# Kernel tuning notes

Hardware: AMD Instinct MI355X
Metric: run time of the kernel (lower is better)

Reference implementation:

```python
import jax, jax.numpy as jnp
import numpy as np

NUM_PAIRS, PAIR_DIM, MACRO_DIM, NUM_SLOTS, BATCH = 28, 128, 256, 64, 4096
D_ALL = NUM_PAIRS * PAIR_DIM  # 3584
EPS = 1e-5


def _layernorm(x, g, b):
    mu = jnp.mean(x, axis=-1, keepdims=True)
    var = jnp.mean(jnp.square(x - mu), axis=-1, keepdims=True)
    return (x - mu) * jax.lax.rsqrt(var + EPS) * g + b


def _memory_read(q, keys, values):
    # attention-style associative read: softmax(q K^T / sqrt(dk)) V
    dk = keys.shape[-1]
    scores = jnp.einsum('bd,sd->bs', q, keys) / jnp.sqrt(jnp.asarray(dk, q.dtype))
    attn = jax.nn.softmax(scores, axis=-1)
    return jnp.einsum('bs,sv->bv', attn, values)


def setup_inputs() -> dict:
    key = jax.random.key(0)
    ks = jax.random.split(key, 12)
    s = lambda k, shape, scale=0.02: jax.random.normal(k, shape, dtype=jnp.float32) * scale
    return {
        'pair_states': jax.random.normal(ks[0], (BATCH, NUM_PAIRS, PAIR_DIM), dtype=jnp.float32),
        'macro_state': jax.random.normal(ks[1], (BATCH, MACRO_DIM), dtype=jnp.float32),
        'mem_pair_keys': s(ks[2], (NUM_SLOTS, PAIR_DIM)),
        'mem_pair_vals': s(ks[3], (NUM_SLOTS, D_ALL)),
        'mem_macro_keys': s(ks[4], (NUM_SLOTS, MACRO_DIM)),
        'mem_macro_vals': s(ks[5], (NUM_SLOTS, D_ALL)),
        'fusion_w1': s(ks[6], (2 * D_ALL, D_ALL)),
        'fusion_b1': jnp.zeros((D_ALL,), jnp.float32),
        'fusion_ln_g': jnp.ones((D_ALL,), jnp.float32),
        'fusion_ln_b': jnp.zeros((D_ALL,), jnp.float32),
        'fusion_w2': s(ks[7], (D_ALL, D_ALL)),
        'fusion_b2': jnp.zeros((D_ALL,), jnp.float32),
        'pair_w': s(ks[8], (NUM_PAIRS, 2 * PAIR_DIM, PAIR_DIM)),
        'pair_b': jnp.zeros((NUM_PAIRS, PAIR_DIM), jnp.float32),
        'pair_ln_g': jnp.ones((NUM_PAIRS, PAIR_DIM), jnp.float32),
        'pair_ln_b': jnp.zeros((NUM_PAIRS, PAIR_DIM), jnp.float32),
    }


def reference(pair_states, macro_state, mem_pair_keys, mem_pair_vals,
              mem_macro_keys, mem_macro_vals, fusion_w1, fusion_b1,
              fusion_ln_g, fusion_ln_b, fusion_w2, fusion_b2,
              pair_w, pair_b, pair_ln_g, pair_ln_b):
    B = pair_states.shape[0]
    # associative memory reads
    pair_query = jnp.mean(pair_states, axis=1)                       # (B, pair_dim)
    pair_corr = _memory_read(pair_query, mem_pair_keys, mem_pair_vals)   # (B, D_ALL)
    macro_corr = _memory_read(macro_state, mem_macro_keys, mem_macro_vals)  # (B, D_ALL)
    # fusion MLP: Linear -> LayerNorm -> GELU -> Linear
    h = jnp.concatenate([pair_corr, macro_corr], axis=-1) @ fusion_w1 + fusion_b1
    h = jax.nn.gelu(_layernorm(h, fusion_ln_g, fusion_ln_b), approximate=False)
    fused = (h @ fusion_w2 + fusion_b2).reshape(B, NUM_PAIRS, PAIR_DIM)
    # per-pair Linear + LayerNorm, batched over the pair axis
    x = jnp.concatenate([pair_states, fused], axis=-1)               # (B, P, 2*pair_dim)
    out = jnp.einsum('bpd,pde->bpe', x, pair_w) + pair_b
    return _layernorm(out, pair_ln_g, pair_ln_b)
```

## Files before the change

kernel.cpp:

```cpp
#include <hip/hip_runtime.h>
#include <hip/hip_bf16.h>
#include <math.h>


#define B_SZ  4096
#define NPAIR 28
#define PDIM  128
#define MDIM  256
#define NSLOT 64
#define DALL  3584
#define DCAT  7168
#define KS2   16
#define KCH2  448

typedef __hip_bfloat16 bf16;
typedef __attribute__((ext_vector_type(8))) short bf16x8;
typedef __attribute__((ext_vector_type(4))) float f32x4;

#define BARRIER() asm volatile("s_barrier" ::: "memory")
#define LGKM0()   asm volatile("s_waitcnt lgkmcnt(0)" ::: "memory")
#define VMCNT4()  asm volatile("s_waitcnt vmcnt(4)" ::: "memory")
#define VMCNT0()  asm volatile("s_waitcnt vmcnt(0)" ::: "memory")

__device__ __forceinline__ void async_copy16(void* lds, const void* g) {
  __builtin_amdgcn_global_load_lds((__attribute__((address_space(1))) void*)g,
                                   (__attribute__((address_space(3))) void*)lds,
                                   16, 0, 0);
}

__global__ __launch_bounds__(512, 2)
void gemm224(const bf16* __restrict__ A, const bf16* __restrict__ Bt,
             bf16* __restrict__ Cout, const float* __restrict__ bias) {
  __shared__ __align__(16) char smem[131072];
  const int tid = threadIdx.x;
  const int wid = tid >> 6, lane = tid & 63;
  const int lr = lane & 15, lk = lane >> 4;
  const int wm = wid >> 1, wn = wid & 1;
  const int swz = ((int)blockIdx.x & 7) * 32 + ((int)blockIdx.x >> 3);
  const int bx = swz & 15, by = swz >> 4;
  const int col0 = bx * 224, row0 = by * 256;

  char* sA = smem;
  char* sB = smem + 65536;

  const int srow = tid >> 3;
  const int sg = (tid & 7) ^ (srow & 7);
  const bf16* aStage = A + (long)(row0 + srow) * DALL + sg * 8;
  const bf16* bStage = Bt + (long)(col0 + srow) * DALL + sg * 8;
  const int wOff = wid << 10;

  const int NT = DALL >> 6;

  const int sx = lr & 7;
  const int arowb = wm * 64 + lr;
  const int browb = wn * 112 + lr;

  f32x4 acc[4][7];
  const f32x4 zero = {0.f, 0.f, 0.f, 0.f};
#pragma unroll
  for (int m = 0; m < 4; ++m)
#pragma unroll
    for (int n = 0; n < 7; ++n) acc[m][n] = zero;

#pragma unroll
  for (int i = 0; i < 4; ++i)
    async_copy16(sB + i * 8192 + wOff, bStage + (long)i * 64 * DALL);
#pragma unroll
  for (int i = 0; i < 4; ++i)
    async_copy16(sA + i * 8192 + wOff, aStage + (long)i * 64 * DALL);
#pragma unroll
  for (int i = 0; i < 4; ++i)
    async_copy16(sB + 32768 + i * 8192 + wOff, bStage + (long)i * 64 * DALL + 64);
  VMCNT4();
  BARRIER();

  bf16x8 af[4][2], bf[7][2];

  for (int t = 0; t < NT; ++t) {
    const int cur = t & 1;
    char* cA = sA + cur * 32768;
    char* cB = sB + cur * 32768;
    char* nA = sA + (cur ^ 1) * 32768;

    if (t + 1 < NT) {
      const bf16* g = aStage + (long)(t + 1) * 64;
#pragma unroll
      for (int i = 0; i < 4; ++i)
        async_copy16(nA + i * 8192 + wOff, g + (long)i * 64 * DALL);
    }
#pragma unroll
    for (int m = 0; m < 4; ++m)
#pragma unroll
      for (int kk = 0; kk < 2; ++kk)
        af[m][kk] = *(const bf16x8*)(cA + (arowb + m * 16) * 128 +
                                     ((((kk << 2) | lk) ^ sx) << 4));
#pragma unroll
    for (int n = 0; n < 7; ++n)
#pragma unroll
      for (int kk = 0; kk < 2; ++kk)
        bf[n][kk] = *(const bf16x8*)(cB + (browb + n * 16) * 128 +
                                     ((((kk << 2) | lk) ^ sx) << 4));
    __builtin_amdgcn_s_setprio(1);
#pragma unroll
    for (int m = 0; m < 4; ++m)
#pragma unroll
      for (int n = 0; n < 4; ++n)
#pragma unroll
        for (int kk = 0; kk < 2; ++kk)
          acc[m][n] = __builtin_amdgcn_mfma_f32_16x16x32_bf16(
              af[m][kk], bf[n][kk], acc[m][n], 0, 0, 0);
    __builtin_amdgcn_s_setprio(0);
    LGKM0();
    BARRIER();

    const int more = (t + 2 < NT);
    if (more) {
      const bf16* g = bStage + (long)(t + 2) * 64;
#pragma unroll
      for (int i = 0; i < 4; ++i)
        async_copy16(cB + i * 8192 + wOff, g + (long)i * 64 * DALL);
    }
    __builtin_amdgcn_s_setprio(1);
#pragma unroll
    for (int m = 0; m < 4; ++m)
#pragma unroll
      for (int n = 4; n < 7; ++n)
#pragma unroll
        for (int kk = 0; kk < 2; ++kk)
          acc[m][n] = __builtin_amdgcn_mfma_f32_16x16x32_bf16(
              af[m][kk], bf[n][kk], acc[m][n], 0, 0, 0);
    __builtin_amdgcn_s_setprio(0);
    if (more) { VMCNT4(); } else { VMCNT0(); }
    BARRIER();
  }

#pragma unroll
  for (int m = 0; m < 4; ++m) {
#pragma unroll
    for (int n = 0; n < 7; ++n) {
      const int gc = col0 + wn * 112 + n * 16 + lr;
      const float bia = bias[gc];
#pragma unroll
      for (int j = 0; j < 4; ++j) {
        const int gr = row0 + wm * 64 + m * 16 + lk * 4 + j;
        Cout[(long)gr * DALL + gc] = __float2bfloat16(acc[m][n][j] + bia);
      }
    }
  }
}

__global__ __launch_bounds__(256)
void tconv_kernel(const float* __restrict__ in, bf16* __restrict__ out,
                  int R, int C, int inBatch, int outBatch) {
  __shared__ float tile[32][33];
  const int tid = threadIdx.x;
  const int tx = tid & 31, ty = tid >> 5;
  const long ib = (long)blockIdx.z * inBatch;
  const long ob = (long)blockIdx.z * outBatch;
  const int c0 = blockIdx.x * 32, r0 = blockIdx.y * 32;
#pragma unroll
  for (int i = 0; i < 4; ++i)
    tile[ty + i * 8][tx] = in[ib + (long)(r0 + ty + i * 8) * C + c0 + tx];
  __syncthreads();
#pragma unroll
  for (int i = 0; i < 4; ++i)
    out[ob + (long)(c0 + ty + i * 8) * R + r0 + tx] =
        __float2bfloat16(tile[tx][ty + i * 8]);
}

__global__ __launch_bounds__(256)
void conv2_kernel(const float* __restrict__ pv, const float* __restrict__ mv,
                  bf16* __restrict__ pvb, bf16* __restrict__ mvb) {
  const float* in = blockIdx.y ? mv : pv;
  bf16* out = blockIdx.y ? mvb : pvb;
  const int i = (blockIdx.x * 256 + threadIdx.x) * 8;
  float4 a = *(const float4*)(in + i);
  float4 b = *(const float4*)(in + i + 4);
  bf16 o[8];
  o[0] = __float2bfloat16(a.x); o[1] = __float2bfloat16(a.y);
  o[2] = __float2bfloat16(a.z); o[3] = __float2bfloat16(a.w);
  o[4] = __float2bfloat16(b.x); o[5] = __float2bfloat16(b.y);
  o[6] = __float2bfloat16(b.z); o[7] = __float2bfloat16(b.w);
  *(bf16x8*)(out + i) = *(bf16x8*)o;
}

__global__ __launch_bounds__(256)
void prep_kernel(const float* __restrict__ ps, const float* __restrict__ mac,
                 const float* __restrict__ pkeys, const float* __restrict__ mkeys,
                 bf16* __restrict__ psb, bf16* __restrict__ att) {
  const int b = blockIdx.x, tid = threadIdx.x;
  __shared__ float q[PDIM];
  __shared__ float mrow[MDIM];
  const float* prow = ps + (long)b * DALL;
  if (tid < MDIM) mrow[tid] = mac[(long)b * MDIM + tid];
  if (tid < PDIM) {
    float s = 0.f;
#pragma unroll
    for (int p = 0; p < NPAIR; ++p) s += prow[p * PDIM + tid];
    q[tid] = s * (1.f / NPAIR);
  }
  for (int i = tid; i < DALL; i += 256)
    psb[(long)b * DALL + i] = __float2bfloat16(prow[i]);
  __syncthreads();
  const int wid = tid >> 6, lane = tid & 63;
  if (wid == 0) {
    float sc = 0.f;
    const float* kr = pkeys + lane * PDIM;
    for (int d = 0; d < PDIM; ++d) sc += q[d] * kr[d];
    sc *= 0.08838834764831845f;
    float mx = sc;
#pragma unroll
    for (int m = 32; m; m >>= 1) mx = fmaxf(mx, __shfl_xor(mx, m));
    float e = expf(sc - mx);
    float ssum = e;
#pragma unroll
    for (int m = 32; m; m >>= 1) ssum += __shfl_xor(ssum, m);
    att[(long)b * 128 + lane] = __float2bfloat16(e / ssum);
  } else if (wid == 1) {
    float sc = 0.f;
    const float* kr = mkeys + lane * MDIM;
    for (int d = 0; d < MDIM; ++d) sc += mrow[d] * kr[d];
    sc *= 0.0625f;
    float mx = sc;
#pragma unroll
    for (int m = 32; m; m >>= 1) mx = fmaxf(mx, __shfl_xor(mx, m));
    float e = expf(sc - mx);
    float ssum = e;
#pragma unroll
    for (int m = 32; m; m >>= 1) ssum += __shfl_xor(ssum, m);
    att[(long)b * 128 + 64 + lane] = __float2bfloat16(e / ssum);
  }
}

__global__ __launch_bounds__(256)
void precompute_direct(const float* __restrict__ w1, const bf16* __restrict__ pvb,
                       const bf16* __restrict__ mvb, float* __restrict__ part) {
  __shared__ __align__(16) bf16 sAt[256 * 40];
  __shared__ __align__(16) bf16 sBt[64 * 32];
  const int tid = threadIdx.x, wid = tid >> 6, lane = tid & 63;
  const int lr = lane & 15, lk = lane >> 4;
  const int n0 = blockIdx.x * 256;
  const int ksb = blockIdx.y;
  const int kbase = ksb * KCH2;
  const bf16* vb = (ksb < 8) ? pvb : mvb;
  const int kcol0 = (ksb < 8) ? kbase : kbase - DALL;

  const int bs = tid >> 2;
  const int bgs = (tid & 3) ^ (bs & 3);

  f32x4 acc[4][4];
  const f32x4 zero = {0.f, 0.f, 0.f, 0.f};
#pragma unroll
  for (int m = 0; m < 4; ++m)
#pragma unroll
    for (int n = 0; n < 4; ++n) acc[m][n] = zero;

  for (int kt = 0; kt < KCH2; kt += 32) {
    __syncthreads();
    {
      const float* src = w1 + (long)(kbase + kt) * DALL + n0 + tid;
      bf16* dst = sAt + tid * 40;
#pragma unroll
      for (int r = 0; r < 32; ++r)
        dst[r] = __float2bfloat16(src[(long)r * DALL]);
    }
    async_copy16((char*)sBt + tid * 16,
                 vb + (long)bs * DALL + kcol0 + kt + bgs * 8);
    __syncthreads();
    bf16x8 af[4], bfr[4];
#pragma unroll
    for (int m = 0; m < 4; ++m)
      af[m] = *(const bf16x8*)((const char*)sAt +
                               ((wid * 64 + m * 16 + lr) * 40 + lk * 8) * 2);
#pragma unroll
    for (int n = 0; n < 4; ++n) {
      const int s = n * 16 + lr;
      bfr[n] = *(const bf16x8*)((const char*)sBt + s * 64 + ((lk ^ (s & 3)) << 4));
    }
#pragma unroll
    for (int m = 0; m < 4; ++m)
#pragma unroll
      for (int n = 0; n < 4; ++n)
        acc[m][n] =
            __builtin_amdgcn_mfma_f32_16x16x32_bf16(af[m], bfr[n], acc[m][n], 0, 0, 0);
  }
#pragma unroll
  for (int m = 0; m < 4; ++m)
#pragma unroll
    for (int n = 0; n < 4; ++n)
#pragma unroll
      for (int j = 0; j < 4; ++j) {
        const int gn = n0 + wid * 64 + m * 16 + lk * 4 + j;
        const int s = n * 16 + lr;
        part[((long)ksb * DALL + gn) * 64 + s] = acc[m][n][j];
      }
}

__global__ __launch_bounds__(256)
void reduce_cvt(const float* __restrict__ part, bf16* __restrict__ cvt) {
  const long i4 = ((long)blockIdx.x * 256 + threadIdx.x) * 4;
  const int n = (int)(i4 >> 7), sc = (int)(i4 & 127);
  const int half = sc >> 6, s0 = sc & 63;
  f32x4 s = {0.f, 0.f, 0.f, 0.f};
#pragma unroll
  for (int j = 0; j < 8; ++j)
    s += *(const f32x4*)(part + ((long)(half * 8 + j) * DALL + n) * 64 + s0);
#pragma unroll
  for (int k = 0; k < 4; ++k) cvt[i4 + k] = __float2bfloat16(s[k]);
}

template <int OUT_BF16, int ADD_BIAS>
__global__ __launch_bounds__(256)
void gemm_bt(const bf16* __restrict__ A, int lda, const bf16* __restrict__ Bt,
             void* __restrict__ Cout, int ldc, int col_off,
             const float* __restrict__ bias, int K) {
  __shared__ __align__(16) bf16 sA[128 * 32];
  __shared__ __align__(16) bf16 sB[128 * 32];
  const int tid = threadIdx.x;
  const int wid = tid >> 6, lane = tid & 63;
  const int lr = lane & 15, lk = lane >> 4;
  const int col0 = blockIdx.x * 128, row0 = blockIdx.y * 128;
  const int wrow = (wid >> 1) * 64, wcol = (wid & 1) * 64;
  const int ea = tid * 8;
  const int ra = ea >> 5, ca = ea & 31;

  f32x4 acc[4][4];
  const f32x4 zero = {0.f, 0.f, 0.f, 0.f};
#pragma unroll
  for (int m = 0; m < 4; ++m)
#pragma unroll
    for (int n = 0; n < 4; ++n) acc[m][n] = zero;

  const long aBase = (long)row0 * lda;
  const long bBase = (long)col0 * K;
  char* sAb = (char*)sA;
  char* sBb = (char*)sB;
  const int wOff = wid * 1024;

  for (int kt = 0; kt < K; kt += 32) {
    __syncthreads();
#pragma unroll
    for (int i = 0; i < 2; ++i) {
      async_copy16(sAb + i * 4096 + wOff,
                   A + aBase + (long)(ra + i * 64) * lda + kt + ca);
      async_copy16(sBb + i * 4096 + wOff,
                   Bt + bBase + (long)(ra + i * 64) * K + kt + ca);
    }
    __syncthreads();
    bf16x8 af[4], bfr[4];
    const bf16x8* pA = (const bf16x8*)sA;
    const bf16x8* pB = (const bf16x8*)sB;
#pragma unroll
    for (int m = 0; m < 4; ++m) af[m] = pA[(wrow + m * 16 + lr) * 4 + lk];
#pragma unroll
    for (int n = 0; n < 4; ++n) bfr[n] = pB[(wcol + n * 16 + lr) * 4 + lk];
#pragma unroll
    for (int m = 0; m < 4; ++m)
#pragma unroll
      for (int n = 0; n < 4; ++n)
        acc[m][n] =
            __builtin_amdgcn_mfma_f32_16x16x32_bf16(af[m], bfr[n], acc[m][n], 0, 0, 0);
  }
#pragma unroll
  for (int m = 0; m < 4; ++m) {
#pragma unroll
    for (int n = 0; n < 4; ++n) {
      const int gcl = col0 + wcol + n * 16 + lr;
      const float bia = ADD_BIAS ? bias[gcl] : 0.f;
#pragma unroll
      for (int j = 0; j < 4; ++j) {
        const int gr = row0 + wrow + m * 16 + lk * 4 + j;
        const float v = acc[m][n][j] + bia;
        const long off = (long)gr * ldc + col_off + gcl;
        if (OUT_BF16)
          ((bf16*)Cout)[off] = __float2bfloat16(v);
        else
          ((float*)Cout)[off] = v;
      }
    }
  }
}

__global__ __launch_bounds__(256)
void ln_gelu_kernel(const bf16* __restrict__ h, const float* __restrict__ g,
                    const float* __restrict__ bb, bf16* __restrict__ h2) {
  const int row = blockIdx.x, tid = threadIdx.x;
  const bf16* x = h + (long)row * DALL;
  float v[14];
  float s1 = 0.f, s2 = 0.f;
#pragma unroll
  for (int i = 0; i < 14; ++i) {
    v[i] = __bfloat162float(x[i * 256 + tid]);
    s1 += v[i];
    s2 += v[i] * v[i];
  }
#pragma unroll
  for (int m = 32; m; m >>= 1) {
    s1 += __shfl_xor(s1, m);
    s2 += __shfl_xor(s2, m);
  }
  __shared__ float r1[4], r2[4];
  const int wid = tid >> 6, lane = tid & 63;
  if (lane == 0) {
    r1[wid] = s1;
    r2[wid] = s2;
  }
  __syncthreads();
  s1 = r1[0] + r1[1] + r1[2] + r1[3];
  s2 = r2[0] + r2[1] + r2[2] + r2[3];
  const float mean = s1 * (1.f / DALL);
  const float var = s2 * (1.f / DALL) - mean * mean;
  const float rstd = rsqrtf(var + 1e-5f);
#pragma unroll
  for (int i = 0; i < 14; ++i) {
    const int c = i * 256 + tid;
    const float y = (v[i] - mean) * rstd * g[c] + bb[c];
    const float ge = 0.5f * y * (1.f + erff(y * 0.7071067811865475f));
    h2[(long)row * DALL + c] = __float2bfloat16(ge);
  }
}

__global__ __launch_bounds__(256)
void pair_final(const bf16* __restrict__ psb, const bf16* __restrict__ fusedb,
                const bf16* __restrict__ pwT, const float* __restrict__ pb,
                const float* __restrict__ lng, const float* __restrict__ lnb,
                float* __restrict__ out) {
  __shared__ __align__(16) bf16 sA[128 * 32];
  __shared__ __align__(16) bf16 sB[128 * 32];
  const int tid = threadIdx.x, wid = tid >> 6, lane = tid & 63;
  const int lr = lane & 15, lk = lane >> 4;
  const int p = blockIdx.y, row0 = blockIdx.x * 128;
  const int ea = tid * 8, ra = ea >> 5, ca = ea & 31;

  f32x4 acc[2][8];
  const f32x4 zero = {0.f, 0.f, 0.f, 0.f};
#pragma unroll
  for (int m = 0; m < 2; ++m)
#pragma unroll
    for (int n = 0; n < 8; ++n) acc[m][n] = zero;

  const bf16* pwp = pwT + (long)p * (PDIM * MDIM);
  char* sAb = (char*)sA;
  char* sBb = (char*)sB;
  const int wOff = wid * 1024;

  for (int kt = 0; kt < MDIM; kt += 32) {
    __syncthreads();
    const bf16* Asrc = (kt < PDIM) ? psb : fusedb;
    const int kc = kt & (PDIM - 1);
#pragma unroll
    for (int i = 0; i < 2; ++i) {
      async_copy16(sAb + i * 4096 + wOff,
                   Asrc + (long)(row0 + ra + i * 64) * DALL + p * PDIM + kc + ca);
      async_copy16(sBb + i * 4096 + wOff, pwp + (ra + i * 64) * MDIM + kt + ca);
    }
    __syncthreads();
    bf16x8 af[2], bfr[8];
    const bf16x8* pA = (const bf16x8*)sA;
    const bf16x8* pB = (const bf16x8*)sB;
#pragma unroll
    for (int m = 0; m < 2; ++m) af[m] = pA[(wid * 32 + m * 16 + lr) * 4 + lk];
#pragma unroll
    for (int n = 0; n < 8; ++n) bfr[n] = pB[(n * 16 + lr) * 4 + lk];
#pragma unroll
    for (int m = 0; m < 2; ++m)
#pragma unroll
      for (int n = 0; n < 8; ++n)
        acc[m][n] =
            __builtin_amdgcn_mfma_f32_16x16x32_bf16(af[m], bfr[n], acc[m][n], 0, 0, 0);
  }
  float g_[8], b_[8], pb_[8];
#pragma unroll
  for (int n = 0; n < 8; ++n) {
    const int c = n * 16 + lr;
    g_[n] = lng[p * PDIM + c];
    b_[n] = lnb[p * PDIM + c];
    pb_[n] = pb[p * PDIM + c];
  }
#pragma unroll
  for (int m = 0; m < 2; ++m) {
#pragma unroll
    for (int j = 0; j < 4; ++j) {
      float vv[8];
      float s1 = 0.f, s2 = 0.f;
#pragma unroll
      for (int n = 0; n < 8; ++n) {
        vv[n] = acc[m][n][j] + pb_[n];
        s1 += vv[n];
        s2 += vv[n] * vv[n];
      }
#pragma unroll
      for (int msk = 1; msk <= 8; msk <<= 1) {
        s1 += __shfl_xor(s1, msk);
        s2 += __shfl_xor(s2, msk);
      }
      const float mean = s1 * (1.f / 128.f);
      const float var = s2 * (1.f / 128.f) - mean * mean;
      const float rstd = rsqrtf(var + 1e-5f);
      const int gr = row0 + wid * 32 + m * 16 + lk * 4 + j;
      float* orow = out + ((long)gr * NPAIR + p) * PDIM;
#pragma unroll
      for (int n = 0; n < 8; ++n)
        orow[n * 16 + lr] = (vv[n] - mean) * rstd * g_[n] + b_[n];
    }
  }
}

extern "C" void kernel_launch(void* const* d_in, const int* in_sizes, int n_in,
                              void* d_out, int out_size, void* d_ws, size_t ws_size,
                              hipStream_t stream) {
  (void)in_sizes; (void)n_in; (void)out_size; (void)ws_size;
  const float* ps   = (const float*)d_in[0];
  const float* mac  = (const float*)d_in[1];
  const float* pkey = (const float*)d_in[2];
  const float* pval = (const float*)d_in[3];
  const float* mkey = (const float*)d_in[4];
  const float* mval = (const float*)d_in[5];
  const float* w1   = (const float*)d_in[6];
  const float* b1   = (const float*)d_in[7];
  const float* lng1 = (const float*)d_in[8];
  const float* lnb1 = (const float*)d_in[9];
  const float* w2   = (const float*)d_in[10];
  const float* b2   = (const float*)d_in[11];
  const float* pw   = (const float*)d_in[12];
  const float* pb   = (const float*)d_in[13];
  const float* plng = (const float*)d_in[14];
  const float* plnb = (const float*)d_in[15];
  float* out = (float*)d_out;

  char* w = (char*)d_ws;
  size_t off = 0;
  auto carve = [&](size_t bytes) {
    char* pp = w + off;
    off += (bytes + 255) & ~(size_t)255;
    return pp;
  };
  bf16* psb   = (bf16*)carve((size_t)B_SZ * DALL * 2);
  bf16* w2t   = (bf16*)carve((size_t)(DALL + 32) * DALL * 2);
  bf16* pvb   = (bf16*)carve((size_t)NSLOT * DALL * 2);
  bf16* mvb   = (bf16*)carve((size_t)NSLOT * DALL * 2);
  bf16* pwTb  = (bf16*)carve((size_t)NPAIR * PDIM * MDIM * 2);
  bf16* att   = (bf16*)carve((size_t)B_SZ * 128 * 2);
  bf16* cvt   = (bf16*)carve((size_t)DALL * 128 * 2);
  float* part = (float*)carve((size_t)KS2 * DALL * 64 * 4);
  bf16* hpreb = (bf16*)carve((size_t)B_SZ * DALL * 2);
  bf16* h2    = (bf16*)carve((size_t)B_SZ * DALL * 2);
  bf16* fusedb = hpreb;

  conv2_kernel<<<dim3(NSLOT * DALL / 2048, 2), 256, 0, stream>>>(pval, mval, pvb, mvb);
  tconv_kernel<<<dim3(DALL / 32, DALL / 32, 1), 256, 0, stream>>>(w2, w2t, DALL, DALL, 0, 0);
  tconv_kernel<<<dim3(PDIM / 32, MDIM / 32, NPAIR), 256, 0, stream>>>(
      pw, pwTb, MDIM, PDIM, MDIM * PDIM, MDIM * PDIM);
  prep_kernel<<<dim3(B_SZ), 256, 0, stream>>>(ps, mac, pkey, mkey, psb, att);
  precompute_direct<<<dim3(DALL / 256, KS2), 256, 0, stream>>>(w1, pvb, mvb, part);
  reduce_cvt<<<dim3(DALL * 128 / 1024), 256, 0, stream>>>(part, cvt);
  gemm_bt<1, 1><<<dim3(DALL / 128, B_SZ / 128), 256, 0, stream>>>(
      att, 128, cvt, hpreb, DALL, 0, b1, 128);
  ln_gelu_kernel<<<dim3(B_SZ), 256, 0, stream>>>(hpreb, lng1, lnb1, h2);
  gemm224<<<dim3(256), 512, 0, stream>>>(h2, w2t, fusedb, b2);
  pair_final<<<dim3(B_SZ / 128, NPAIR), 256, 0, stream>>>(
      psb, fusedb, pwTb, pb, plng, plnb, out);
}
```

Before: 283.9 us.

## Vectorize bf16 stores and use 64-wide swizzled K tiles in thin GEMMs

Several conversion kernels (tconv, prep, precompute_direct's LDS fill) now pack bf16 values and write 8- or 16-byte vectors instead of scalar 2-byte stores. The generic gemm_bt for the K=128 attention-times-correction GEMM is replaced by a specialized gemm_thin using 64-wide K tiles with an XOR-swizzled LDS layout, halving the number of barrier-separated iterations. pair_final gets the same 64-wide swizzled tiling. The aim is fewer memory transactions, fewer LDS bank conflicts and less synchronization overhead, at the cost of larger LDS footprint per block.

```diff
diff --git a/kernel.cpp b/kernel.cpp
--- a/kernel.cpp
+++ b/kernel.cpp
@@ -15,6 +15,7 @@
 
 typedef __hip_bfloat16 bf16;
 typedef __attribute__((ext_vector_type(8))) short bf16x8;
+typedef __attribute__((ext_vector_type(4))) short short4v;
 typedef __attribute__((ext_vector_type(4))) float f32x4;
 
 #define BARRIER() asm volatile("s_barrier" ::: "memory")
@@ -162,10 +163,11 @@
   for (int i = 0; i < 4; ++i)
     tile[ty + i * 8][tx] = in[ib + (long)(r0 + ty + i * 8) * C + c0 + tx];
   __syncthreads();
-#pragma unroll
-  for (int i = 0; i < 4; ++i)
-    out[ob + (long)(c0 + ty + i * 8) * R + r0 + tx] =
-        __float2bfloat16(tile[tx][ty + i * 8]);
+  const int cl = tid >> 3, rq = (tid & 7) * 4;
+  union { bf16 h[4]; short4v v; } u;
+#pragma unroll
+  for (int j = 0; j < 4; ++j) u.h[j] = __float2bfloat16(tile[rq + j][cl]);
+  *(short4v*)(out + ob + (long)(c0 + cl) * R + r0 + rq) = u.v;
 }
 
 __global__ __launch_bounds__(256)
@@ -176,12 +178,12 @@
   const int i = (blockIdx.x * 256 + threadIdx.x) * 8;
   float4 a = *(const float4*)(in + i);
   float4 b = *(const float4*)(in + i + 4);
-  bf16 o[8];
-  o[0] = __float2bfloat16(a.x); o[1] = __float2bfloat16(a.y);
-  o[2] = __float2bfloat16(a.z); o[3] = __float2bfloat16(a.w);
-  o[4] = __float2bfloat16(b.x); o[5] = __float2bfloat16(b.y);
-  o[6] = __float2bfloat16(b.z); o[7] = __float2bfloat16(b.w);
-  *(bf16x8*)(out + i) = *(bf16x8*)o;
+  union { bf16 h[8]; bf16x8 v; } u;
+  u.h[0] = __float2bfloat16(a.x); u.h[1] = __float2bfloat16(a.y);
+  u.h[2] = __float2bfloat16(a.z); u.h[3] = __float2bfloat16(a.w);
+  u.h[4] = __float2bfloat16(b.x); u.h[5] = __float2bfloat16(b.y);
+  u.h[6] = __float2bfloat16(b.z); u.h[7] = __float2bfloat16(b.w);
+  *(bf16x8*)(out + i) = u.v;
 }
 
 __global__ __launch_bounds__(256)
@@ -199,8 +201,16 @@
     for (int p = 0; p < NPAIR; ++p) s += prow[p * PDIM + tid];
     q[tid] = s * (1.f / NPAIR);
   }
-  for (int i = tid; i < DALL; i += 256)
-    psb[(long)b * DALL + i] = __float2bfloat16(prow[i]);
+  for (int i = tid * 8; i < DALL; i += 2048) {
+    float4 a = *(const float4*)(prow + i);
+    float4 c = *(const float4*)(prow + i + 4);
+    union { bf16 h[8]; bf16x8 v; } u;
+    u.h[0] = __float2bfloat16(a.x); u.h[1] = __float2bfloat16(a.y);
+    u.h[2] = __float2bfloat16(a.z); u.h[3] = __float2bfloat16(a.w);
+    u.h[4] = __float2bfloat16(c.x); u.h[5] = __float2bfloat16(c.y);
+    u.h[6] = __float2bfloat16(c.z); u.h[7] = __float2bfloat16(c.w);
+    *(bf16x8*)(psb + (long)b * DALL + i) = u.v;
+  }
   __syncthreads();
   const int wid = tid >> 6, lane = tid & 63;
   if (wid == 0) {
@@ -261,8 +271,13 @@
       const float* src = w1 + (long)(kbase + kt) * DALL + n0 + tid;
       bf16* dst = sAt + tid * 40;
 #pragma unroll
-      for (int r = 0; r < 32; ++r)
-        dst[r] = __float2bfloat16(src[(long)r * DALL]);
+      for (int r8 = 0; r8 < 32; r8 += 4) {
+        union { bf16 h[4]; short4v v; } u;
+#pragma unroll
+        for (int j = 0; j < 4; ++j)
+          u.h[j] = __float2bfloat16(src[(long)(r8 + j) * DALL]);
+        *(short4v*)(dst + r8) = u.v;
+      }
     }
     async_copy16((char*)sBt + tid * 16,
                  vb + (long)bs * DALL + kcol0 + kt + bgs * 8);
@@ -309,73 +324,64 @@
   for (int k = 0; k < 4; ++k) cvt[i4 + k] = __float2bfloat16(s[k]);
 }
 
-template <int OUT_BF16, int ADD_BIAS>
-__global__ __launch_bounds__(256)
-void gemm_bt(const bf16* __restrict__ A, int lda, const bf16* __restrict__ Bt,
-             void* __restrict__ Cout, int ldc, int col_off,
-             const float* __restrict__ bias, int K) {
-  __shared__ __align__(16) bf16 sA[128 * 32];
-  __shared__ __align__(16) bf16 sB[128 * 32];
-  const int tid = threadIdx.x;
-  const int wid = tid >> 6, lane = tid & 63;
+__global__ __launch_bounds__(256)
+void gemm_thin(const bf16* __restrict__ att, const bf16* __restrict__ cvt,
+               bf16* __restrict__ hpre, const float* __restrict__ bias) {
+  __shared__ __align__(16) bf16 sA[128 * 64];
+  __shared__ __align__(16) bf16 sB[128 * 64];
+  const int tid = threadIdx.x, wid = tid >> 6, lane = tid & 63;
   const int lr = lane & 15, lk = lane >> 4;
   const int col0 = blockIdx.x * 128, row0 = blockIdx.y * 128;
-  const int wrow = (wid >> 1) * 64, wcol = (wid & 1) * 64;
-  const int ea = tid * 8;
-  const int ra = ea >> 5, ca = ea & 31;
-
-  f32x4 acc[4][4];
+  const int srl = lane >> 3;
+  const int sgl = (lane & 7) ^ srl;
+  const int sx = lr & 7;
+
+  f32x4 acc[2][8];
   const f32x4 zero = {0.f, 0.f, 0.f, 0.f};
 #pragma unroll
-  for (int m = 0; m < 4; ++m)
-#pragma unroll
-    for (int n = 0; n < 4; ++n) acc[m][n] = zero;
-
-  const long aBase = (long)row0 * lda;
-  const long bBase = (long)col0 * K;
-  char* sAb = (char*)sA;
-  char* sBb = (char*)sB;
-  const int wOff = wid * 1024;
-
-  for (int kt = 0; kt < K; kt += 32) {
+  for (int m = 0; m < 2; ++m)
+#pragma unroll
+    for (int n = 0; n < 8; ++n) acc[m][n] = zero;
+
+  for (int kt = 0; kt < 2; ++kt) {
     __syncthreads();
 #pragma unroll
-    for (int i = 0; i < 2; ++i) {
-      async_copy16(sAb + i * 4096 + wOff,
-                   A + aBase + (long)(ra + i * 64) * lda + kt + ca);
-      async_copy16(sBb + i * 4096 + wOff,
-                   Bt + bBase + (long)(ra + i * 64) * K + kt + ca);
+    for (int i = 0; i < 4; ++i) {
+      const int r = i * 32 + wid * 8 + srl;
+      async_copy16((char*)sA + i * 4096 + wid * 1024,
+                   att + (long)(row0 + r) * 128 + kt * 64 + sgl * 8);
+      async_copy16((char*)sB + i * 4096 + wid * 1024,
+                   cvt + (long)(col0 + r) * 128 + kt * 64 + sgl * 8);
     }
     __syncthreads();
-    bf16x8 af[4], bfr[4];
-    const bf16x8* pA = (const bf16x8*)sA;
-    const bf16x8* pB = (const bf16x8*)sB;
-#pragma unroll
-    for (int m = 0; m < 4; ++m) af[m] = pA[(wrow + m * 16 + lr) * 4 + lk];
-#pragma unroll
-    for (int n = 0; n < 4; ++n) bfr[n] = pB[(wcol + n * 16 + lr) * 4 + lk];
-#pragma unroll
-    for (int m = 0; m < 4; ++m)
-#pragma unroll
-      for (int n = 0; n < 4; ++n)
-        acc[m][n] =
-            __builtin_amdgcn_mfma_f32_16x16x32_bf16(af[m], bfr[n], acc[m][n], 0, 0, 0);
-  }
-#pragma unroll
-  for (int m = 0; m < 4; ++m) {
-#pragma unroll
-    for (int n = 0; n < 4; ++n) {
-      const int gcl = col0 + wcol + n * 16 + lr;
-      const float bia = ADD_BIAS ? bias[gcl] : 0.f;
+#pragma unroll
+    for (int kk = 0; kk < 2; ++kk) {
+      bf16x8 a0[2], b0[8];
+      const int gb = (((kk << 2) | lk) ^ sx) << 4;
+#pragma unroll
+      for (int m = 0; m < 2; ++m)
+        a0[m] = *(const bf16x8*)((const char*)sA + (wid * 32 + m * 16 + lr) * 128 + gb);
+#pragma unroll
+      for (int n = 0; n < 8; ++n)
+        b0[n] = *(const bf16x8*)((const char*)sB + (n * 16 + lr) * 128 + gb);
+#pragma unroll
+      for (int m = 0; m < 2; ++m)
+#pragma unroll
+        for (int n = 0; n < 8; ++n)
+          acc[m][n] = __builtin_amdgcn_mfma_f32_16x16x32_bf16(
+              a0[m], b0[n], acc[m][n], 0, 0, 0);
+    }
+  }
+#pragma unroll
+  for (int m = 0; m < 2; ++m) {
+#pragma unroll
+    for (int n = 0; n < 8; ++n) {
+      const int gc = col0 + n * 16 + lr;
+      const float bia = bias[gc];
 #pragma unroll
       for (int j = 0; j < 4; ++j) {
-        const int gr = row0 + wrow + m * 16 + lk * 4 + j;
-        const float v = acc[m][n][j] + bia;
-        const long off = (long)gr * ldc + col_off + gcl;
-        if (OUT_BF16)
-          ((bf16*)Cout)[off] = __float2bfloat16(v);
-        else
-          ((float*)Cout)[off] = v;
+        const int gr = row0 + wid * 32 + m * 16 + lk * 4 + j;
+        hpre[(long)gr * DALL + gc] = __float2bfloat16(acc[m][n][j] + bia);
       }
     }
   }
@@ -425,12 +431,15 @@
                 const bf16* __restrict__ pwT, const float* __restrict__ pb,
                 const float* __restrict__ lng, const float* __restrict__ lnb,
                 float* __restrict__ out) {
-  __shared__ __align__(16) bf16 sA[128 * 32];
-  __shared__ __align__(16) bf16 sB[128 * 32];
+  __shared__ __align__(16) bf16 sA[128 * 64];
+  __shared__ __align__(16) bf16 sB[128 * 64];
   const int tid = threadIdx.x, wid = tid >> 6, lane = tid & 63;
   const int lr = lane & 15, lk = lane >> 4;
   const int p = blockIdx.y, row0 = blockIdx.x * 128;
-  const int ea = tid * 8, ra = ea >> 5, ca = ea & 31;
+  const int srl = lane >> 3;
+  const int sgl = (lane & 7) ^ srl;
+  const int sx = lr & 7;
+  const bf16* pwp = pwT + (long)p * (PDIM * MDIM);
 
   f32x4 acc[2][8];
   const f32x4 zero = {0.f, 0.f, 0.f, 0.f};
@@ -439,35 +448,36 @@
 #pragma unroll
     for (int n = 0; n < 8; ++n) acc[m][n] = zero;
 
-  const bf16* pwp = pwT + (long)p * (PDIM * MDIM);
-  char* sAb = (char*)sA;
-  char* sBb = (char*)sB;
-  const int wOff = wid * 1024;
-
-  for (int kt = 0; kt < MDIM; kt += 32) {
+  for (int kt = 0; kt < 4; ++kt) {
     __syncthreads();
-    const bf16* Asrc = (kt < PDIM) ? psb : fusedb;
-    const int kc = kt & (PDIM - 1);
-#pragma unroll
-    for (int i = 0; i < 2; ++i) {
-      async_copy16(sAb + i * 4096 + wOff,
-                   Asrc + (long)(row0 + ra + i * 64) * DALL + p * PDIM + kc + ca);
-      async_copy16(sBb + i * 4096 + wOff, pwp + (ra + i * 64) * MDIM + kt + ca);
+    const bf16* Asrc = (kt < 2) ? psb : fusedb;
+    const int acol = p * PDIM + (kt & 1) * 64;
+#pragma unroll
+    for (int i = 0; i < 4; ++i) {
+      const int r = i * 32 + wid * 8 + srl;
+      async_copy16((char*)sA + i * 4096 + wid * 1024,
+                   Asrc + (long)(row0 + r) * DALL + acol + sgl * 8);
+      async_copy16((char*)sB + i * 4096 + wid * 1024,
+                   pwp + (long)r * MDIM + kt * 64 + sgl * 8);
     }
     __syncthreads();
-    bf16x8 af[2], bfr[8];
-    const bf16x8* pA = (const bf16x8*)sA;
-    const bf16x8* pB = (const bf16x8*)sB;
-#pragma unroll
-    for (int m = 0; m < 2; ++m) af[m] = pA[(wid * 32 + m * 16 + lr) * 4 + lk];
-#pragma unroll
-    for (int n = 0; n < 8; ++n) bfr[n] = pB[(n * 16 + lr) * 4 + lk];
-#pragma unroll
-    for (int m = 0; m < 2; ++m)
+#pragma unroll
+    for (int kk = 0; kk < 2; ++kk) {
+      bf16x8 a0[2], b0[8];
+      const int gb = (((kk << 2) | lk) ^ sx) << 4;
+#pragma unroll
+      for (int m = 0; m < 2; ++m)
+        a0[m] = *(const bf16x8*)((const char*)sA + (wid * 32 + m * 16 + lr) * 128 + gb);
 #pragma unroll
       for (int n = 0; n < 8; ++n)
-        acc[m][n] =
-            __builtin_amdgcn_mfma_f32_16x16x32_bf16(af[m], bfr[n], acc[m][n], 0, 0, 0);
+        b0[n] = *(const bf16x8*)((const char*)sB + (n * 16 + lr) * 128 + gb);
+#pragma unroll
+      for (int m = 0; m < 2; ++m)
+#pragma unroll
+        for (int n = 0; n < 8; ++n)
+          acc[m][n] = __builtin_amdgcn_mfma_f32_16x16x32_bf16(
+              a0[m], b0[n], acc[m][n], 0, 0, 0);
+    }
   }
   float g_[8], b_[8], pb_[8];
 #pragma unroll
@@ -554,8 +564,7 @@
   prep_kernel<<<dim3(B_SZ), 256, 0, stream>>>(ps, mac, pkey, mkey, psb, att);
   precompute_direct<<<dim3(DALL / 256, KS2), 256, 0, stream>>>(w1, pvb, mvb, part);
   reduce_cvt<<<dim3(DALL * 128 / 1024), 256, 0, stream>>>(part, cvt);
-  gemm_bt<1, 1><<<dim3(DALL / 128, B_SZ / 128), 256, 0, stream>>>(
-      att, 128, cvt, hpreb, DALL, 0, b1, 128);
+  gemm_thin<<<dim3(DALL / 128, B_SZ / 128), 256, 0, stream>>>(att, cvt, hpreb, b1);
   ln_gelu_kernel<<<dim3(B_SZ), 256, 0, stream>>>(hpreb, lng1, lnb1, h2);
   gemm224<<<dim3(256), 512, 0, stream>>>(h2, w2t, fusedb, b2);
   pair_final<<<dim3(B_SZ / 128, NPAIR), 256, 0, stream>>>(
```

New measurement: 285.0 us. Within noise of the previous version (+0.4%).
